# Kernel optimization log

Measured on AMD Instinct MI355X. Metric: run time of the kernel, lower is better.

## Reference

```python
import jax, jax.numpy as jnp
import numpy as np

B, S1, S2 = 4, 2048, 2048
IN1, IN2 = 512, 512
KD, VD, H = 64, 64, 8


def setup_inputs() -> dict:
    key = jax.random.key(0)
    ks = jax.random.split(key, 7)
    x1 = jax.random.normal(ks[0], (B, S1, IN1), dtype=jnp.float32)
    x2 = jax.random.normal(ks[1], (B, S2, IN2), dtype=jnp.float32)
    # nn.Linear weights stored as [out, in]; kaiming-uniform-ish scale
    Wq = jax.random.normal(ks[2], (KD * H, IN1), dtype=jnp.float32) * (1.0 / np.sqrt(IN1))
    Wk = jax.random.normal(ks[3], (KD * H, IN2), dtype=jnp.float32) * (1.0 / np.sqrt(IN2))
    Wv = jax.random.normal(ks[4], (VD * H, IN2), dtype=jnp.float32) * (1.0 / np.sqrt(IN2))
    Wo = jax.random.normal(ks[5], (IN1, VD * H), dtype=jnp.float32) * (1.0 / np.sqrt(VD * H))
    bo = jax.random.normal(ks[6], (IN1,), dtype=jnp.float32) * 0.01
    return {"x1": x1, "x2": x2, "Wq": Wq, "Wk": Wk, "Wv": Wv, "Wo": Wo, "bo": bo}


def reference(x1, x2, Wq, Wk, Wv, Wo, bo):
    b, s1, _ = x1.shape
    s2 = x2.shape[1]
    # projections -> [B, H, S, D]
    q = (x1 @ Wq.T).reshape(b, s1, H, KD).transpose(0, 2, 1, 3)
    k = (x2 @ Wk.T).reshape(b, s2, H, KD).transpose(0, 2, 1, 3)
    v = (x2 @ Wv.T).reshape(b, s2, H, VD).transpose(0, 2, 1, 3)
    # scores [B, H, S1, S2]
    attn = jnp.einsum('bhqd,bhkd->bhqk', q, k) / jnp.sqrt(jnp.float32(KD))
    attn = jax.nn.softmax(attn, axis=-1)
    out = jnp.einsum('bhqk,bhkd->bhqd', attn, v)  # [B, H, S1, VD]
    out = out.transpose(0, 2, 1, 3).reshape(b, s1, H * VD)
    return out @ Wo.T + bo
```

## Files before the change

### kernel.cpp

```cpp
#include <hip/hip_runtime.h>
#include <stdint.h>

typedef __bf16 bf16;
typedef __bf16 bf16x8 __attribute__((ext_vector_type(8)));
typedef __bf16 bf16x4 __attribute__((ext_vector_type(4)));
typedef float f32x4 __attribute__((ext_vector_type(4)));
typedef float f32x16 __attribute__((ext_vector_type(16)));
typedef uint32_t u32x4 __attribute__((ext_vector_type(4)));

#define MFMA16x16x32(A, B, C) __builtin_amdgcn_mfma_f32_16x16x32_bf16((A), (B), (C), 0, 0, 0)
#define MFMA32x32x16(A, B, C) __builtin_amdgcn_mfma_f32_32x32x16_bf16((A), (B), (C), 0, 0, 0)
#define SBAR() do { __builtin_amdgcn_s_barrier(); __builtin_amdgcn_sched_barrier(0); } while (0)

__device__ __forceinline__ void gload_lds16(const void* g, void* l) {
  __builtin_amdgcn_global_load_lds((const __attribute__((address_space(1))) void*)g,
                                   (__attribute__((address_space(3))) void*)l,
                                   16, 0, 0);
}

__device__ __forceinline__ float fexp2(float x) { return __builtin_amdgcn_exp2f(x); }

__device__ __forceinline__ uint32_t cvtpk(float a, float b) {
  uint32_t r;
  asm("v_cvt_pk_bf16_f32 %0, %1, %2" : "=v"(r) : "v"(a), "v"(b));
  return r;
}
__device__ __forceinline__ void plswap(uint32_t& a, uint32_t& b) {
  asm volatile("v_permlane32_swap_b32 %0, %1" : "+v"(a), "+v"(b));
}

__device__ __forceinline__ bf16x8 cvt8(float4 a, float4 b) {
  bf16x8 o;
  o[0] = (bf16)a.x; o[1] = (bf16)a.y; o[2] = (bf16)a.z; o[3] = (bf16)a.w;
  o[4] = (bf16)b.x; o[5] = (bf16)b.y; o[6] = (bf16)b.z; o[7] = (bf16)b.w;
  return o;
}

__global__ void cast_x(const float* __restrict__ x1, const float* __restrict__ x2,
                       const float* __restrict__ Wq, const float* __restrict__ Wk,
                       const float* __restrict__ Wv, const float* __restrict__ Wo,
                       bf16* __restrict__ out) {
  const size_t i = ((size_t)blockIdx.x * blockDim.x + threadIdx.x) * 8;
  const float* src;
  if      (i < 4194304u) src = x1 + i;
  else if (i < 8388608u) src = x2 + (i - 4194304u);
  else if (i < 8650752u) src = Wq + (i - 8388608u);
  else if (i < 8912896u) src = Wk + (i - 8650752u);
  else if (i < 9175040u) src = Wv + (i - 8912896u);
  else                   src = Wo + (i - 9175040u);
  float4 a = *reinterpret_cast<const float4*>(src);
  float4 b = *reinterpret_cast<const float4*>(src + 4);
  *reinterpret_cast<bf16x8*>(out + i) = cvt8(a, b);
}

__global__ __launch_bounds__(256, 3) void qkv128_kernel(
    const bf16* __restrict__ x1b, const bf16* __restrict__ x2b,
    const bf16* __restrict__ Wb, bf16* __restrict__ Qw,
    bf16* __restrict__ Kw, bf16* __restrict__ Vtw) {
  __shared__ bf16 As[3][128 * 32];
  __shared__ bf16 Bs[3][128 * 32];
  const int tid = threadIdx.x;
  const int w = tid >> 6, l = tid & 63;
  const int wr = w >> 1, wc = w & 1;
  const int lr = l & 15, lg = l >> 4;
  const int bm = blockIdx.x, bn = blockIdx.y;
  const int K = 512;
  const int sel = bn >> 2, wn = bn & 3;

  const bf16* A = (sel == 0) ? x1b : x2b;
  const bf16* B = Wb + (size_t)sel * 262144 + (size_t)wn * 128 * K;

  const int c_row = l >> 2;
  const int sw = ((l & 3) ^ (c_row & 3)) * 8;

  auto stage = [&](int t, int bb) {
#pragma unroll
    for (int i = 0; i < 2; i++) {
      const int q = w + i * 4;
      gload_lds16(A + (size_t)(bm * 128 + q * 16 + c_row) * K + t * 32 + sw, &As[bb][q * 512]);
      gload_lds16(B + (size_t)(q * 16 + c_row) * K + t * 32 + sw, &Bs[bb][q * 512]);
    }
  };

  f32x4 acc[4][4] = {};
  const int swz = (lr & 3) * 8;

  stage(0, 0);
  stage(1, 1);
  asm volatile("s_waitcnt vmcnt(4)" ::: "memory");
  SBAR();

  const int NT = 16;
  for (int t = 0; t < NT; t++) {
    if (t + 2 < NT) stage(t + 2, (t + 2) % 3);
    const int cur = t % 3;
    bf16x8 a[4], b[4];
#pragma unroll
    for (int mi = 0; mi < 4; mi++)
      a[mi] = *reinterpret_cast<const bf16x8*>(
          &As[cur][(wr * 64 + mi * 16 + lr) * 32 + (lg * 8 ^ swz)]);
#pragma unroll
    for (int ni = 0; ni < 4; ni++)
      b[ni] = *reinterpret_cast<const bf16x8*>(
          &Bs[cur][(wc * 64 + ni * 16 + lr) * 32 + (lg * 8 ^ swz)]);
#pragma unroll
    for (int mi = 0; mi < 4; mi++)
#pragma unroll
      for (int ni = 0; ni < 4; ni++)
        acc[mi][ni] = MFMA16x16x32(a[mi], b[ni], acc[mi][ni]);

    if (t + 1 < NT) {
      if (t + 2 < NT) asm volatile("s_waitcnt vmcnt(4)" ::: "memory");
      else            asm volatile("s_waitcnt vmcnt(0)" ::: "memory");
      asm volatile("s_waitcnt lgkmcnt(0)" ::: "memory");
      SBAR();
    }
  }

  const float scale = (sel == 0) ? 0.18033688011112f : 1.0f;
#pragma unroll
  for (int mi = 0; mi < 4; mi++) {
    const int m0 = bm * 128 + wr * 64 + mi * 16 + lg * 4;
#pragma unroll
    for (int ni = 0; ni < 4; ni++) {
      const int gn = wn * 128 + wc * 64 + ni * 16 + lr;
      if (sel < 2) {
        bf16* dst = (sel == 0) ? Qw : Kw;
#pragma unroll
        for (int r = 0; r < 4; r++) {
          const int m = m0 + r;
          size_t d = (size_t)((m >> 11) * 8 + (gn >> 6)) * 131072 + (size_t)(m & 2047) * 64 + (gn & 63);
          dst[d] = (bf16)(acc[mi][ni][r] * scale);
        }
      } else {
        bf16x4 pv;
#pragma unroll
        for (int r = 0; r < 4; r++) pv[r] = (bf16)acc[mi][ni][r];
        size_t base = ((size_t)(m0 >> 11) * 512 + gn) * 2048 + (m0 & 2047);
        *reinterpret_cast<bf16x4*>(Vtw + base) = pv;
      }
    }
  }
}

__global__ __launch_bounds__(256, 4) void outproj_kernel(
    const bf16* __restrict__ A0, const float* __restrict__ W0,
    float* __restrict__ C0, const float* __restrict__ bias) {
  __shared__ bf16 As[3][128 * 32];
  __shared__ bf16 Bs[2][64 * 32];
  const int tid = threadIdx.x;
  const int w = tid >> 6, l = tid & 63;
  const int wr = w >> 1, wc = w & 1;
  const int lr = l & 15, lg = l >> 4;
  const int bm = blockIdx.x, bn = blockIdx.y;
  const int K = 512;

  const float* Bf = W0 + (size_t)bn * 64 * K;
  const int c_row = l >> 2;
  const int c_s = l & 3;
  const int sw = (c_s ^ (c_row & 3)) * 8;

  float4 lb[2][2];
  auto issue_A = [&](int t, int bb) {
#pragma unroll
    for (int i = 0; i < 2; i++) {
      const int q = w + i * 4;
      gload_lds16(A0 + (size_t)(bm * 128 + q * 16 + c_row) * K + t * 32 + sw, &As[bb][q * 512]);
    }
  };
  auto issue_B = [&](int t, int s) {
    const float* pb = Bf + (size_t)(w * 16 + c_row) * K + t * 32 + c_s * 8;
    lb[s][0] = *reinterpret_cast<const float4*>(pb);
    lb[s][1] = *reinterpret_cast<const float4*>(pb + 4);
  };
  auto commit_B = [&](int s, int bb) {
    *reinterpret_cast<bf16x8*>(&Bs[bb][w * 512 + c_row * 32 + sw]) = cvt8(lb[s][0], lb[s][1]);
  };

  f32x4 acc[4][2] = {};
  const int swz = (lr & 3) * 8;

  issue_A(0, 0); issue_B(0, 0);
  issue_A(1, 1); issue_B(1, 1);
  asm volatile("s_waitcnt vmcnt(4)" ::: "memory");
  commit_B(0, 0);
  asm volatile("s_waitcnt lgkmcnt(0)" ::: "memory");
  SBAR();

  const int NT = 16;
  for (int t = 0; t < NT; t++) {
    if (t + 2 < NT) { issue_A(t + 2, (t + 2) % 3); issue_B(t + 2, t & 1); }

    bf16x8 a[4], b[2];
    const int cur = t % 3;
#pragma unroll
    for (int mi = 0; mi < 4; mi++)
      a[mi] = *reinterpret_cast<const bf16x8*>(
          &As[cur][(wr * 64 + mi * 16 + lr) * 32 + (lg * 8 ^ swz)]);
#pragma unroll
    for (int ni = 0; ni < 2; ni++)
      b[ni] = *reinterpret_cast<const bf16x8*>(
          &Bs[t & 1][(wc * 32 + ni * 16 + lr) * 32 + (lg * 8 ^ swz)]);
#pragma unroll
    for (int mi = 0; mi < 4; mi++)
#pragma unroll
      for (int ni = 0; ni < 2; ni++)
        acc[mi][ni] = MFMA16x16x32(a[mi], b[ni], acc[mi][ni]);

    if (t + 1 < NT) {
      if (t + 2 < NT) asm volatile("s_waitcnt vmcnt(4)" ::: "memory");
      else            asm volatile("s_waitcnt vmcnt(0)" ::: "memory");
      commit_B((t + 1) & 1, (t + 1) & 1);
      asm volatile("s_waitcnt lgkmcnt(0)" ::: "memory");
      SBAR();
    }
  }

#pragma unroll
  for (int mi = 0; mi < 4; mi++) {
    const int m0 = bm * 128 + wr * 64 + mi * 16 + lg * 4;
#pragma unroll
    for (int ni = 0; ni < 2; ni++) {
      const int gn = bn * 64 + wc * 32 + ni * 16 + lr;
      const float bv = bias[gn];
#pragma unroll
      for (int r = 0; r < 4; r++)
        C0[(size_t)(m0 + r) * 512 + gn] = acc[mi][ni][r] + bv;
    }
  }
}

__global__ __launch_bounds__(512, 2) void attn_kernel(
    const bf16* __restrict__ Q, const bf16* __restrict__ Kk,
    const bf16* __restrict__ Vt, bf16* __restrict__ AO) {
  __shared__ bf16 KV[2][2][64 * 64];
  __shared__ float ls[4][32];

  const int tid = threadIdx.x;
  const int w = tid >> 6, l = tid & 63;
  const int q32 = l & 31;
  const int h = l >> 5;
  const int qg = w >> 1, kvh = w & 1;

  const int lin = blockIdx.x;
  const int xcd = lin & 7;
  const int m = lin >> 3;
  const int bh = xcd * 4 + (m & 3);
  const int qb = m >> 2;
  const int b = bh >> 3, hd = bh & 7;

  const bf16* Qb = Q + (size_t)bh * 131072;
  const bf16* Kb = Kk + (size_t)bh * 131072;
  const bf16* Vb = Vt + (size_t)bh * 131072;

  const int q0 = qb * 128 + qg * 32;

  bf16x8 qf[4];
#pragma unroll
  for (int ks = 0; ks < 4; ks++)
    qf[ks] = *reinterpret_cast<const bf16x8*>(
        Qb + (size_t)(q0 + q32) * 64 + ks * 16 + h * 8);

  const int crow = l >> 3;
  const int scol = ((l & 7) ^ crow) * 8;
  auto stage = [&](int kv0, int bb) {
    const int row = w * 8 + crow;
    gload_lds16(Kb + (size_t)(kv0 + row) * 64 + scol, &KV[0][bb][w * 512]);
    gload_lds16(Vb + (size_t)row * 2048 + kv0 + scol, &KV[1][bb][w * 512]);
  };

  f32x16 oacc[2] = {};
  float lsum = 0.f;
  const int l7 = l & 7;

  stage(0, 0);
  asm volatile("s_waitcnt vmcnt(0)" ::: "memory");
  SBAR();

  for (int t = 0; t < 32; t++) {
    const int cur = t & 1;
    if (t < 31) stage((t + 1) * 64, cur ^ 1);

    bf16x8 kb[4];
#pragma unroll
    for (int ks = 0; ks < 4; ks++)
      kb[ks] = *reinterpret_cast<const bf16x8*>(
          &KV[0][cur][(kvh * 32 + q32) * 64 + (((ks * 2 + h) ^ l7) * 8)]);

    f32x16 st = {};
#pragma unroll
    for (int ks = 0; ks < 4; ks++)
      st = MFMA32x32x16(kb[ks], qf[ks], st);

    float e[16];
#pragma unroll
    for (int r = 0; r < 16; r++) {
      e[r] = fexp2(st[r]);
      lsum += e[r];
    }
    uint32_t Qp[8];
#pragma unroll
    for (int p = 0; p < 8; p++) Qp[p] = cvtpk(e[2 * p], e[2 * p + 1]);
    plswap(Qp[0], Qp[2]);
    plswap(Qp[1], Qp[3]);
    plswap(Qp[4], Qp[6]);
    plswap(Qp[5], Qp[7]);
    const bf16x8 pa0 = __builtin_bit_cast(bf16x8, (u32x4){Qp[0], Qp[1], Qp[2], Qp[3]});
    const bf16x8 pa1 = __builtin_bit_cast(bf16x8, (u32x4){Qp[4], Qp[5], Qp[6], Qp[7]});

#pragma unroll
    for (int kst = 0; kst < 2; kst++) {
      const bf16x8 pa = (kst == 0) ? pa0 : pa1;
#pragma unroll
      for (int db = 0; db < 2; db++) {
        bf16x8 vb = *reinterpret_cast<const bf16x8*>(
            &KV[1][cur][(db * 32 + q32) * 64 + (((kvh * 4 + kst * 2 + h) ^ l7) * 8)]);
        oacc[db] = MFMA32x32x16(pa, vb, oacc[db]);
      }
    }

    if (t < 31) {
      asm volatile("s_waitcnt vmcnt(0) lgkmcnt(0)" ::: "memory");
      SBAR();
    }
  }

  lsum += __shfl_xor(lsum, 32);

  float* cb = (float*)&KV[0][0][0];
  __syncthreads();
  if (kvh == 1) {
#pragma unroll
    for (int db = 0; db < 2; db++)
#pragma unroll
      for (int r = 0; r < 16; r++)
        cb[((qg * 4 + db * 2 + (r >> 3)) * 8 + (r & 7)) * 64 + l] = oacc[db][r];
    if (l < 32) ls[qg][q32] = lsum;
  }
  __syncthreads();
  if (kvh == 0) {
    lsum += ls[qg][q32];
#pragma unroll
    for (int db = 0; db < 2; db++)
#pragma unroll
      for (int r = 0; r < 16; r++)
        oacc[db][r] += cb[((qg * 4 + db * 2 + (r >> 3)) * 8 + (r & 7)) * 64 + l];

    float inv[16];
#pragma unroll
    for (int r = 0; r < 16; r++) {
      const int qv = (r & 3) + 8 * (r >> 2) + 4 * h;
      inv[r] = 1.f / __shfl(lsum, qv);
    }
#pragma unroll
    for (int db = 0; db < 2; db++) {
#pragma unroll
      for (int r = 0; r < 16; r++) {
        const int qv = (r & 3) + 8 * (r >> 2) + 4 * h;
        AO[(size_t)(b * 2048 + q0 + qv) * 512 + hd * 64 + db * 32 + q32] =
            (bf16)(oacc[db][r] * inv[r]);
      }
    }
  }
}

extern "C" void kernel_launch(void* const* d_in, const int* in_sizes, int n_in,
                              void* d_out, int out_size, void* d_ws, size_t ws_size,
                              hipStream_t stream) {
  (void)in_sizes; (void)n_in; (void)out_size; (void)ws_size;
  const float* x1 = (const float*)d_in[0];
  const float* x2 = (const float*)d_in[1];
  const float* Wq = (const float*)d_in[2];
  const float* Wk = (const float*)d_in[3];
  const float* Wv = (const float*)d_in[4];
  const float* Wo = (const float*)d_in[5];
  const float* bo = (const float*)d_in[6];

  uint8_t* ws = (uint8_t*)d_ws;
  bf16* x1b = (bf16*)(ws + 0);
  bf16* x2b = (bf16*)(ws + 8388608);
  bf16* Wsb = (bf16*)(ws + 16777216);
  bf16* AO  = (bf16*)(ws + 0);
  bf16* Qws = (bf16*)(ws + 18874368);
  bf16* Kws = (bf16*)(ws + 27262976);
  bf16* Vtw = (bf16*)(ws + 35651584);

  cast_x<<<4608, 256, 0, stream>>>(x1, x2, Wq, Wk, Wv, Wo, x1b);

  qkv128_kernel<<<dim3(64, 12), 256, 0, stream>>>(x1b, x2b, Wsb, Qws, Kws, Vtw);

  attn_kernel<<<512, 512, 0, stream>>>(Qws, Kws, Vtw, AO);

  outproj_kernel<<<dim3(64, 8), 256, 0, stream>>>(AO, Wo, (float*)d_out, bo);
}
```

Before: 98.26 us.

## Double query rows per attention block to reuse K/V tiles across two Q subtiles

Each wave now handles two 32-row query subtiles instead of one, so every staged K and V tile in LDS feeds twice as many MFMAs. Grid size halves to 256 blocks and launch bounds drop to one block per CU to allow the extra accumulator registers. The split-KV reduction at the end is done in two passes to fit the scratch buffer. Per-block K/V global traffic is amortized, at the cost of fewer blocks than CUs (256 on a 256-CU part) and lower occupancy for latency hiding.

```diff
diff --git a/kernel.cpp b/kernel.cpp
--- a/kernel.cpp
+++ b/kernel.cpp
@@ -230,11 +230,11 @@
   }
 }
 
-__global__ __launch_bounds__(512, 2) void attn_kernel(
+__global__ __launch_bounds__(512, 1) void attn_kernel(
     const bf16* __restrict__ Q, const bf16* __restrict__ Kk,
     const bf16* __restrict__ Vt, bf16* __restrict__ AO) {
   __shared__ bf16 KV[2][2][64 * 64];
-  __shared__ float ls[4][32];
+  __shared__ float cls[4][2][32];
 
   const int tid = threadIdx.x;
   const int w = tid >> 6, l = tid & 63;
@@ -253,13 +253,15 @@
   const bf16* Kb = Kk + (size_t)bh * 131072;
   const bf16* Vb = Vt + (size_t)bh * 131072;
 
-  const int q0 = qb * 128 + qg * 32;
-
-  bf16x8 qf[4];
-#pragma unroll
-  for (int ks = 0; ks < 4; ks++)
-    qf[ks] = *reinterpret_cast<const bf16x8*>(
-        Qb + (size_t)(q0 + q32) * 64 + ks * 16 + h * 8);
+  const int q0 = qb * 256 + qg * 64;
+
+  bf16x8 qf[2][4];
+#pragma unroll
+  for (int i = 0; i < 2; i++)
+#pragma unroll
+    for (int ks = 0; ks < 4; ks++)
+      qf[i][ks] = *reinterpret_cast<const bf16x8*>(
+          Qb + (size_t)(q0 + i * 32 + q32) * 64 + ks * 16 + h * 8);
 
   const int crow = l >> 3;
   const int scol = ((l & 7) ^ crow) * 8;
@@ -269,8 +271,8 @@
     gload_lds16(Vb + (size_t)row * 2048 + kv0 + scol, &KV[1][bb][w * 512]);
   };
 
-  f32x16 oacc[2] = {};
-  float lsum = 0.f;
+  f32x16 oacc[2][2] = {};
+  float lsum[2] = {0.f, 0.f};
   const int l7 = l & 7;
 
   stage(0, 0);
@@ -287,37 +289,46 @@
       kb[ks] = *reinterpret_cast<const bf16x8*>(
           &KV[0][cur][(kvh * 32 + q32) * 64 + (((ks * 2 + h) ^ l7) * 8)]);
 
-    f32x16 st = {};
-#pragma unroll
-    for (int ks = 0; ks < 4; ks++)
-      st = MFMA32x32x16(kb[ks], qf[ks], st);
-
-    float e[16];
-#pragma unroll
-    for (int r = 0; r < 16; r++) {
-      e[r] = fexp2(st[r]);
-      lsum += e[r];
-    }
-    uint32_t Qp[8];
-#pragma unroll
-    for (int p = 0; p < 8; p++) Qp[p] = cvtpk(e[2 * p], e[2 * p + 1]);
-    plswap(Qp[0], Qp[2]);
-    plswap(Qp[1], Qp[3]);
-    plswap(Qp[4], Qp[6]);
-    plswap(Qp[5], Qp[7]);
-    const bf16x8 pa0 = __builtin_bit_cast(bf16x8, (u32x4){Qp[0], Qp[1], Qp[2], Qp[3]});
-    const bf16x8 pa1 = __builtin_bit_cast(bf16x8, (u32x4){Qp[4], Qp[5], Qp[6], Qp[7]});
-
-#pragma unroll
-    for (int kst = 0; kst < 2; kst++) {
-      const bf16x8 pa = (kst == 0) ? pa0 : pa1;
-#pragma unroll
-      for (int db = 0; db < 2; db++) {
-        bf16x8 vb = *reinterpret_cast<const bf16x8*>(
+    bf16x8 pa[2][2];
+#pragma unroll
+    for (int i = 0; i < 2; i++) {
+      f32x16 st = {};
+#pragma unroll
+      for (int ks = 0; ks < 4; ks++)
+        st = MFMA32x32x16(kb[ks], qf[i][ks], st);
+
+      float e[16];
+#pragma unroll
+      for (int r = 0; r < 16; r++) {
+        e[r] = fexp2(st[r]);
+        lsum[i] += e[r];
+      }
+      uint32_t Qp[8];
+#pragma unroll
+      for (int p = 0; p < 8; p++) Qp[p] = cvtpk(e[2 * p], e[2 * p + 1]);
+      plswap(Qp[0], Qp[2]);
+      plswap(Qp[1], Qp[3]);
+      plswap(Qp[4], Qp[6]);
+      plswap(Qp[5], Qp[7]);
+      pa[i][0] = __builtin_bit_cast(bf16x8, (u32x4){Qp[0], Qp[1], Qp[2], Qp[3]});
+      pa[i][1] = __builtin_bit_cast(bf16x8, (u32x4){Qp[4], Qp[5], Qp[6], Qp[7]});
+    }
+
+    bf16x8 vb[2][2];
+#pragma unroll
+    for (int kst = 0; kst < 2; kst++)
+#pragma unroll
+      for (int db = 0; db < 2; db++)
+        vb[kst][db] = *reinterpret_cast<const bf16x8*>(
             &KV[1][cur][(db * 32 + q32) * 64 + (((kvh * 4 + kst * 2 + h) ^ l7) * 8)]);
-        oacc[db] = MFMA32x32x16(pa, vb, oacc[db]);
-      }
-    }
+
+#pragma unroll
+    for (int i = 0; i < 2; i++)
+#pragma unroll
+      for (int kst = 0; kst < 2; kst++)
+#pragma unroll
+        for (int db = 0; db < 2; db++)
+          oacc[i][db] = MFMA32x32x16(pa[i][kst], vb[kst][db], oacc[i][db]);
 
     if (t < 31) {
       asm volatile("s_waitcnt vmcnt(0) lgkmcnt(0)" ::: "memory");
@@ -325,40 +336,53 @@
     }
   }
 
-  lsum += __shfl_xor(lsum, 32);
+#pragma unroll
+  for (int i = 0; i < 2; i++) lsum[i] += __shfl_xor(lsum[i], 32);
 
   float* cb = (float*)&KV[0][0][0];
   __syncthreads();
-  if (kvh == 1) {
-#pragma unroll
-    for (int db = 0; db < 2; db++)
-#pragma unroll
-      for (int r = 0; r < 16; r++)
-        cb[((qg * 4 + db * 2 + (r >> 3)) * 8 + (r & 7)) * 64 + l] = oacc[db][r];
-    if (l < 32) ls[qg][q32] = lsum;
-  }
-  __syncthreads();
+  if (kvh == 1 && l < 32) {
+    cls[qg][0][q32] = lsum[0];
+    cls[qg][1][q32] = lsum[1];
+  }
+#pragma unroll
+  for (int i = 0; i < 2; i++) {
+    if (kvh == 1) {
+#pragma unroll
+      for (int db = 0; db < 2; db++)
+#pragma unroll
+        for (int r = 0; r < 16; r++)
+          cb[((qg * 2 + db) * 16 + r) * 64 + l] = oacc[i][db][r];
+    }
+    __syncthreads();
+    if (kvh == 0) {
+#pragma unroll
+      for (int db = 0; db < 2; db++)
+#pragma unroll
+        for (int r = 0; r < 16; r++)
+          oacc[i][db][r] += cb[((qg * 2 + db) * 16 + r) * 64 + l];
+    }
+    __syncthreads();
+  }
+
   if (kvh == 0) {
-    lsum += ls[qg][q32];
-#pragma unroll
-    for (int db = 0; db < 2; db++)
-#pragma unroll
-      for (int r = 0; r < 16; r++)
-        oacc[db][r] += cb[((qg * 4 + db * 2 + (r >> 3)) * 8 + (r & 7)) * 64 + l];
-
-    float inv[16];
-#pragma unroll
-    for (int r = 0; r < 16; r++) {
-      const int qv = (r & 3) + 8 * (r >> 2) + 4 * h;
-      inv[r] = 1.f / __shfl(lsum, qv);
-    }
-#pragma unroll
-    for (int db = 0; db < 2; db++) {
+#pragma unroll
+    for (int i = 0; i < 2; i++) {
+      lsum[i] += cls[qg][i][q32];
+      float inv[16];
 #pragma unroll
       for (int r = 0; r < 16; r++) {
         const int qv = (r & 3) + 8 * (r >> 2) + 4 * h;
-        AO[(size_t)(b * 2048 + q0 + qv) * 512 + hd * 64 + db * 32 + q32] =
-            (bf16)(oacc[db][r] * inv[r]);
+        inv[r] = 1.f / __shfl(lsum[i], qv);
+      }
+#pragma unroll
+      for (int db = 0; db < 2; db++) {
+#pragma unroll
+        for (int r = 0; r < 16; r++) {
+          const int qv = (r & 3) + 8 * (r >> 2) + 4 * h;
+          AO[(size_t)(b * 2048 + q0 + i * 32 + qv) * 512 + hd * 64 + db * 32 + q32] =
+              (bf16)(oacc[i][db][r] * inv[r]);
+        }
       }
     }
   }
@@ -389,7 +413,7 @@
 
   qkv128_kernel<<<dim3(64, 12), 256, 0, stream>>>(x1b, x2b, Wsb, Qws, Kws, Vtw);
 
-  attn_kernel<<<512, 512, 0, stream>>>(Qws, Kws, Vtw, AO);
+  attn_kernel<<<256, 512, 0, stream>>>(Qws, Kws, Vtw, AO);
 
   outproj_kernel<<<dim3(64, 8), 256, 0, stream>>>(AO, Wo, (float*)d_out, bo);
 }
```

New measurement: 97.01 us. No clear change (-1.3%).
